# Kernel tuning notes

Measured on AMD Instinct MI355X. Metric: run time of the kernel, lower is better.

## Reference

```python
import jax, jax.numpy as jnp
import numpy as np

# DCNv2 config (matches init_kwargs)
STRIDE, PAD, DIL = 1, 1, 1
KH, KW = 3, 3
K = KH * KW


def setup_inputs() -> dict:
    key = jax.random.key(0)
    k1, k2, k3, k4 = jax.random.split(key, 4)
    B, C, H, W = 2, 256, 96, 96
    O = 256
    inp = jax.random.normal(k1, (B, C, H, W), jnp.float32)
    # offset channels interleaved (dy, dx) per kernel tap -> 2*K channels
    offset = jax.random.normal(k2, (B, 2 * K, H, W), jnp.float32)
    # modulation mask in [0,1) (sigmoid is applied outside this module in DCN heads)
    mask = jax.random.uniform(k3, (B, K, H, W), jnp.float32)
    n = C * KH * KW
    stdv = 1.0 / float(np.sqrt(n))
    weight = jax.random.uniform(k4, (O, C, KH, KW), jnp.float32, -stdv, stdv)
    bias = jnp.zeros((O,), jnp.float32)
    return {"input": inp, "offset": offset, "mask": mask, "weight": weight, "bias": bias}


def reference(input, offset, mask, weight, bias):
    B, C, H, W = input.shape
    O = weight.shape[0]
    Ho = (H + 2 * PAD - DIL * (KH - 1) - 1) // STRIDE + 1
    Wo = (W + 2 * PAD - DIL * (KW - 1) - 1) // STRIDE + 1

    # learned per-pixel offsets: channel layout [dy_k0, dx_k0, dy_k1, dx_k1, ...]
    dy = offset[:, 0::2]  # [B,K,Ho,Wo]
    dx = offset[:, 1::2]  # [B,K,Ho,Wo]

    ky = (jnp.arange(K) // KW * DIL).astype(jnp.float32)  # kernel tap row offsets
    kx = (jnp.arange(K) % KW * DIL).astype(jnp.float32)   # kernel tap col offsets
    base_y = (jnp.arange(Ho) * STRIDE - PAD).astype(jnp.float32)
    base_x = (jnp.arange(Wo) * STRIDE - PAD).astype(jnp.float32)

    # sampling positions, [B,K,Ho,Wo]
    y = base_y[None, None, :, None] + ky[None, :, None, None] + dy
    x = base_x[None, None, None, :] + kx[None, :, None, None] + dx

    y0 = jnp.floor(y)
    x0 = jnp.floor(x)
    wy = y - y0  # bilinear fractional weights
    wx = x - x0

    inp_flat = input.reshape(B, C, H * W)

    def gather(yi, xi):
        # zero-padded bilinear corner gather: out-of-bounds -> 0
        ii = yi.astype(jnp.int32)
        jj = xi.astype(jnp.int32)
        valid = ((ii >= 0) & (ii < H) & (jj >= 0) & (jj < W)).astype(input.dtype)
        idx = jnp.clip(ii, 0, H - 1) * W + jnp.clip(jj, 0, W - 1)  # [B,K,Ho,Wo]
        v = jnp.take_along_axis(inp_flat, idx.reshape(B, 1, -1), axis=2)  # [B,C,K*Ho*Wo]
        return v * valid.reshape(B, 1, -1)

    v00 = gather(y0, x0)
    v01 = gather(y0, x0 + 1)
    v10 = gather(y0 + 1, x0)
    v11 = gather(y0 + 1, x0 + 1)

    wyf = wy.reshape(B, 1, -1)
    wxf = wx.reshape(B, 1, -1)
    sampled = (v00 * (1 - wyf) * (1 - wxf) + v01 * (1 - wyf) * wxf
               + v10 * wyf * (1 - wxf) + v11 * wyf * wxf)  # [B,C,K*Ho*Wo]

    mod = sampled * mask.reshape(B, 1, -1)           # modulation per tap/pixel
    mod = mod.reshape(B, C, K, Ho * Wo)
    out = jnp.einsum('bcks,ock->bos', mod, weight.reshape(O, C, K)) + bias[None, :, None]
    return out.reshape(B, O, Ho, Wo)
```

## Files before the change

kernel.cpp:

```cpp
#include <hip/hip_runtime.h>
#include <hip/hip_bf16.h>


#define Hh 96
#define Ww 96
#define Cc 256
#define Oo 256
#define Bb 2
#define Kk 9
#define Ss (Hh * Ww)
#define CKTOT (Cc * Kk)

typedef __bf16 bf16x8 __attribute__((ext_vector_type(8)));
typedef __bf16 bf16x2v __attribute__((ext_vector_type(2)));
typedef float f32x16 __attribute__((ext_vector_type(16)));
typedef float f32x2 __attribute__((ext_vector_type(2)));

__device__ __forceinline__ f32x2 up2(unsigned u) {
  f32x2 r;
  r.x = __uint_as_float(u << 16);
  r.y = __uint_as_float(u & 0xffff0000u);
  return r;
}

__device__ __forceinline__ void barrier_lgkm() {
  asm volatile("" ::: "memory");
  __builtin_amdgcn_s_waitcnt(0xC07F);
  __builtin_amdgcn_s_barrier();
  asm volatile("" ::: "memory");
}

__global__ __launch_bounds__(256) void prep(const float* __restrict__ inp,
                                            const float* __restrict__ wsrc,
                                            __bf16* __restrict__ it,
                                            __bf16* __restrict__ wt) {
  __shared__ float tile[64][65];
  const int bx = blockIdx.x;
  const int tid = threadIdx.x;

  if (bx < 1152) {
    const int hw0 = (bx % 144) * 64;
    const int c0 = ((bx / 144) & 3) * 64;
    const int b = bx / 576;
    const int hw_l = tid & 63, cr = tid >> 6;
    const float* src = inp + ((size_t)(b * Cc + c0) * Ss) + hw0;
#pragma unroll
    for (int r = 0; r < 16; ++r) {
      int c_l = r * 4 + cr;
      tile[c_l][hw_l] = src[(size_t)c_l * Ss + hw_l];
    }
    __syncthreads();
    const int cp = (tid & 31) * 2, hr = tid >> 5;
    __bf16* dst = it + ((size_t)(b * Ss + hw0) * Cc) + c0;
#pragma unroll
    for (int r = 0; r < 8; ++r) {
      int hw_s = r * 8 + hr;
      bf16x2v p;
      p.x = (__bf16)tile[cp][hw_s];
      p.y = (__bf16)tile[cp + 1][hw_s];
      *(bf16x2v*)(dst + (size_t)hw_s * Cc + cp) = p;
    }
  } else {
    int i = (bx - 1152) * 256 + tid;
    int j = i & 7;
    int l = (i >> 3) & 63;
    int osub = (i >> 9) & 7;
    int cc = (i >> 12) & 15;
    int kk = i >> 16;
    int o = osub * 32 + (l & 31);
    int ch = cc * 16 + ((l >> 5) << 3) + j;
    wt[i] = (__bf16)wsrc[(o * Cc + ch) * Kk + kk];
  }
}

__global__ __launch_bounds__(256, 3) void dcn_main(
    const __bf16* __restrict__ it,
    const __bf16* __restrict__ wt,
    const float* __restrict__ offset,
    const float* __restrict__ mask,
    const float* __restrict__ bias,
    float* __restrict__ out)
{
  __shared__ __bf16 colT[2][32 * 256];
  __shared__ int4 pa9[9][32];
  __shared__ float4 pw9[9][32];

  const int tid = threadIdx.x;
  const int tile = (blockIdx.x & 7) * 36 + (blockIdx.x >> 3);
  const int s0 = tile * 32;
  const int b = blockIdx.y;
  const int lane = tid & 63;
  const int wv = tid >> 6;
  const int sB = lane & 31;
  const int hi = lane >> 5;
  const int fs = tid >> 3;
  const int fg = tid & 7;

  const __bf16* itb = it + (size_t)b * Ss * Cc;

  for (int idx = tid; idx < 9 * 32; idx += 256) {
    int kk = idx >> 5;
    int sl = idx & 31;
    int s = s0 + sl;
    int ho = s / Ww;
    int wo = s - ho * Ww;
    float dy = offset[((size_t)(b * 18 + 2 * kk)) * Ss + s];
    float dx = offset[((size_t)(b * 18 + 2 * kk + 1)) * Ss + s];
    float m = mask[((size_t)(b * 9 + kk)) * Ss + s];
    float y = (float)(ho - 1 + kk / 3) + dy;
    float x = (float)(wo - 1 + kk % 3) + dx;
    float fy = floorf(y), fx = floorf(x);
    int y0 = (int)fy, x0 = (int)fx;
    float wy = y - fy, wx = x - fx;
    int y1 = y0 + 1, x1 = x0 + 1;
    float vy0 = (y0 >= 0 && y0 < Hh) ? 1.f : 0.f;
    float vy1 = (y1 >= 0 && y1 < Hh) ? 1.f : 0.f;
    float vx0 = (x0 >= 0 && x0 < Ww) ? 1.f : 0.f;
    float vx1 = (x1 >= 0 && x1 < Ww) ? 1.f : 0.f;
    int y0c = min(max(y0, 0), Hh - 1), y1c = min(max(y1, 0), Hh - 1);
    int x0c = min(max(x0, 0), Ww - 1), x1c = min(max(x1, 0), Ww - 1);
    pa9[kk][sl] = make_int4((y0c * Ww + x0c) * Cc, (y0c * Ww + x1c) * Cc,
                            (y1c * Ww + x0c) * Cc, (y1c * Ww + x1c) * Cc);
    pw9[kk][sl] = make_float4(m * (1.f - wy) * (1.f - wx) * vy0 * vx0,
                              m * (1.f - wy) * wx * vy0 * vx1,
                              m * wy * (1.f - wx) * vy1 * vx0,
                              m * wy * wx * vy1 * vx1);
  }
  __syncthreads();

  f32x16 acc0, acc1;
#pragma unroll
  for (int j = 0; j < 16; ++j) { acc0[j] = 0.f; acc1[j] = 0.f; }

  auto ldW = [&](int kk, int cc, int which) {
    size_t idx = (size_t)((kk * 16 + cc) * 8 + wv * 2 + which);
    return *(const bf16x8*)(wt + (idx << 9) + (lane << 3));
  };
  auto ldB = [&](int buf, int cc) {
    int g = ((2 * cc + hi) ^ (sB & 7)) << 3;
    return *(const bf16x8*)(&colT[buf][sB * 256 + g]);
  };

  for (int kk = 0; kk < Kk; ++kk) {
    const int buf = kk & 1;
    {
      int4 a = pa9[kk][fs];
      float4 wq = pw9[kk][fs];
      __bf16* drow = &colT[buf][fs * 256];
#pragma unroll
      for (int it2 = 0; it2 < 4; ++it2) {
        int g = fg + it2 * 8;
        const __bf16* p = itb + g * 8;
        uint4 c00 = *(const uint4*)(p + a.x);
        uint4 c01 = *(const uint4*)(p + a.y);
        uint4 c10 = *(const uint4*)(p + a.z);
        uint4 c11 = *(const uint4*)(p + a.w);
        unsigned u0[4] = {c00.x, c00.y, c00.z, c00.w};
        unsigned u1[4] = {c01.x, c01.y, c01.z, c01.w};
        unsigned u2[4] = {c10.x, c10.y, c10.z, c10.w};
        unsigned u3[4] = {c11.x, c11.y, c11.z, c11.w};
        bf16x8 rv;
#pragma unroll
        for (int w = 0; w < 4; ++w) {
          f32x2 r = up2(u0[w]) * wq.x + up2(u1[w]) * wq.y +
                    up2(u2[w]) * wq.z + up2(u3[w]) * wq.w;
          rv[2 * w] = (__bf16)r.x;
          rv[2 * w + 1] = (__bf16)r.y;
        }
        *(bf16x8*)(drow + ((g ^ (fs & 7)) << 3)) = rv;
      }
    }
    bf16x8 Wacur = ldW(kk, 0, 0);
    bf16x8 Wbcur = ldW(kk, 0, 1);
    barrier_lgkm();

    bf16x8 Bcur = ldB(buf, 0);
#pragma unroll
    for (int cc = 0; cc < 16; ++cc) {
      bf16x8 Bn, Wan, Wbn;
      if (cc < 15) {
        Bn = ldB(buf, cc + 1);
        Wan = ldW(kk, cc + 1, 0);
        Wbn = ldW(kk, cc + 1, 1);
      }
      acc0 = __builtin_amdgcn_mfma_f32_32x32x16_bf16(Wacur, Bcur, acc0, 0, 0, 0);
      acc1 = __builtin_amdgcn_mfma_f32_32x32x16_bf16(Wbcur, Bcur, acc1, 0, 0, 0);
      if (cc < 15) {
        Bcur = Bn;
        Wacur = Wan;
        Wbcur = Wbn;
      }
    }
  }

  float* ob = out + (size_t)b * Oo * Ss + s0 + sB;
#pragma unroll
  for (int os = 0; os < 2; ++os) {
#pragma unroll
    for (int r = 0; r < 16; ++r) {
      int o = wv * 64 + os * 32 + (r & 3) + 8 * (r >> 2) + 4 * hi;
      float v = (os ? acc1[r] : acc0[r]) + bias[o];
      ob[(size_t)o * Ss] = v;
    }
  }
}

extern "C" void kernel_launch(void* const* d_in, const int* in_sizes, int n_in,
                              void* d_out, int out_size, void* d_ws, size_t ws_size,
                              hipStream_t stream) {
  (void)in_sizes; (void)n_in; (void)out_size; (void)ws_size;
  const float* inp = (const float*)d_in[0];
  const float* offset = (const float*)d_in[1];
  const float* mask = (const float*)d_in[2];
  const float* weight = (const float*)d_in[3];
  const float* bias = (const float*)d_in[4];
  float* out = (float*)d_out;

  __bf16* it = (__bf16*)d_ws;
  __bf16* wt = (__bf16*)((char*)d_ws + (size_t)Bb * Ss * Cc * 2);

  prep<<<3456, 256, 0, stream>>>(inp, weight, it, wt);
  dcn_main<<<dim3(288, Bb), 256, 0, stream>>>(it, wt, offset, mask, bias, out);
}
```

Measured before the change: 128.1 us.

## Software-pipeline bilinear gather of next tap with MFMA of current tap

Restructures the main loop so the bilinear gather and blend for tap kk+1 is issued in two halves, interleaved with the MFMA chain for tap kk, writing into the other LDS buffer. This hides global gather latency behind matrix math and removes the per-tap serialization of gather then compute. Operand prefetch depth for weights and B fragments is raised to three steps ahead. Occupancy is dropped from 3 to 2 waves per SIMD to make room for the extra live registers, which could reduce latency hiding elsewhere.

```diff
diff --git a/kernel.cpp b/kernel.cpp
--- a/kernel.cpp
+++ b/kernel.cpp
@@ -73,7 +73,42 @@
   }
 }
 
-__global__ __launch_bounds__(256, 3) void dcn_main(
+__device__ __forceinline__ void issue_half(const __bf16* __restrict__ itb,
+                                           const int4 a, int fg, int h,
+                                           uint4 (&c)[2][4]) {
+#pragma unroll
+  for (int t = 0; t < 2; ++t) {
+    const __bf16* p = itb + (fg + (h * 2 + t) * 8) * 8;
+    c[t][0] = *(const uint4*)(p + a.x);
+    c[t][1] = *(const uint4*)(p + a.y);
+    c[t][2] = *(const uint4*)(p + a.z);
+    c[t][3] = *(const uint4*)(p + a.w);
+  }
+}
+
+__device__ __forceinline__ void proc_half(const float4 wq, int fg, int fs, int h,
+                                          const uint4 (&c)[2][4],
+                                          __bf16* __restrict__ drow) {
+#pragma unroll
+  for (int t = 0; t < 2; ++t) {
+    int g = fg + (h * 2 + t) * 8;
+    unsigned u0[4] = {c[t][0].x, c[t][0].y, c[t][0].z, c[t][0].w};
+    unsigned u1[4] = {c[t][1].x, c[t][1].y, c[t][1].z, c[t][1].w};
+    unsigned u2[4] = {c[t][2].x, c[t][2].y, c[t][2].z, c[t][2].w};
+    unsigned u3[4] = {c[t][3].x, c[t][3].y, c[t][3].z, c[t][3].w};
+    bf16x8 rv;
+#pragma unroll
+    for (int w = 0; w < 4; ++w) {
+      f32x2 r = up2(u0[w]) * wq.x + up2(u1[w]) * wq.y +
+                up2(u2[w]) * wq.z + up2(u3[w]) * wq.w;
+      rv[2 * w] = (__bf16)r.x;
+      rv[2 * w + 1] = (__bf16)r.y;
+    }
+    *(bf16x8*)(drow + ((g ^ (fs & 7)) << 3)) = rv;
+  }
+}
+
+__global__ __launch_bounds__(256, 2) void dcn_main(
     const __bf16* __restrict__ it,
     const __bf16* __restrict__ wt,
     const float* __restrict__ offset,
@@ -141,57 +176,66 @@
     return *(const bf16x8*)(&colT[buf][sB * 256 + g]);
   };
 
+  bf16x8 Wa[4], Wb[4], Bv[4];
+  uint4 cA[2][4], cB[2][4];
+
+  {
+    int4 a0 = pa9[0][fs];
+    float4 w0 = pw9[0][fs];
+    issue_half(itb, a0, fg, 0, cA);
+    issue_half(itb, a0, fg, 1, cB);
+    proc_half(w0, fg, fs, 0, cA, &colT[0][fs * 256]);
+    proc_half(w0, fg, fs, 1, cB, &colT[0][fs * 256]);
+  }
+  Wa[0] = ldW(0, 0, 0); Wb[0] = ldW(0, 0, 1);
+  Wa[1] = ldW(0, 1, 0); Wb[1] = ldW(0, 1, 1);
+  barrier_lgkm();
+
+#define STEP(cc)                                                               \
+  {                                                                            \
+    if ((cc) < 13) {                                                           \
+      Wa[((cc) + 3) & 3] = ldW(kk, (cc) + 3, 0);                               \
+      Wb[((cc) + 3) & 3] = ldW(kk, (cc) + 3, 1);                               \
+      Bv[((cc) + 3) & 3] = ldB(buf, (cc) + 3);                                 \
+    }                                                                          \
+    acc0 = __builtin_amdgcn_mfma_f32_32x32x16_bf16(Wa[(cc) & 3], Bv[(cc) & 3], \
+                                                   acc0, 0, 0, 0);             \
+    acc1 = __builtin_amdgcn_mfma_f32_32x32x16_bf16(Wb[(cc) & 3], Bv[(cc) & 3], \
+                                                   acc1, 0, 0, 0);             \
+  }
+
   for (int kk = 0; kk < Kk; ++kk) {
     const int buf = kk & 1;
-    {
-      int4 a = pa9[kk][fs];
-      float4 wq = pw9[kk][fs];
-      __bf16* drow = &colT[buf][fs * 256];
-#pragma unroll
-      for (int it2 = 0; it2 < 4; ++it2) {
-        int g = fg + it2 * 8;
-        const __bf16* p = itb + g * 8;
-        uint4 c00 = *(const uint4*)(p + a.x);
-        uint4 c01 = *(const uint4*)(p + a.y);
-        uint4 c10 = *(const uint4*)(p + a.z);
-        uint4 c11 = *(const uint4*)(p + a.w);
-        unsigned u0[4] = {c00.x, c00.y, c00.z, c00.w};
-        unsigned u1[4] = {c01.x, c01.y, c01.z, c01.w};
-        unsigned u2[4] = {c10.x, c10.y, c10.z, c10.w};
-        unsigned u3[4] = {c11.x, c11.y, c11.z, c11.w};
-        bf16x8 rv;
-#pragma unroll
-        for (int w = 0; w < 4; ++w) {
-          f32x2 r = up2(u0[w]) * wq.x + up2(u1[w]) * wq.y +
-                    up2(u2[w]) * wq.z + up2(u3[w]) * wq.w;
-          rv[2 * w] = (__bf16)r.x;
-          rv[2 * w + 1] = (__bf16)r.y;
-        }
-        *(bf16x8*)(drow + ((g ^ (fs & 7)) << 3)) = rv;
-      }
-    }
-    bf16x8 Wacur = ldW(kk, 0, 0);
-    bf16x8 Wbcur = ldW(kk, 0, 1);
+    int4 na;
+    float4 nwq;
+    if (kk < 8) {
+      na = pa9[kk + 1][fs];
+      issue_half(itb, na, fg, 0, cA);
+    }
+    Bv[0] = ldB(buf, 0);
+    Bv[1] = ldB(buf, 1);
+    Bv[2] = ldB(buf, 2);
+    Wa[2] = ldW(kk, 2, 0);
+    Wb[2] = ldW(kk, 2, 1);
+
+    STEP(0) STEP(1) STEP(2) STEP(3) STEP(4) STEP(5) STEP(6) STEP(7)
+
+    if (kk < 8) {
+      nwq = pw9[kk + 1][fs];
+      proc_half(nwq, fg, fs, 0, cA, &colT[buf ^ 1][fs * 256]);
+      issue_half(itb, na, fg, 1, cB);
+    }
+
+    STEP(8) STEP(9) STEP(10) STEP(11) STEP(12) STEP(13) STEP(14) STEP(15)
+
+    if (kk < 8) {
+      proc_half(nwq, fg, fs, 1, cB, &colT[buf ^ 1][fs * 256]);
+      Wa[0] = ldW(kk + 1, 0, 0); Wb[0] = ldW(kk + 1, 0, 1);
+      Wa[1] = ldW(kk + 1, 1, 0); Wb[1] = ldW(kk + 1, 1, 1);
+    }
     barrier_lgkm();
-
-    bf16x8 Bcur = ldB(buf, 0);
-#pragma unroll
-    for (int cc = 0; cc < 16; ++cc) {
-      bf16x8 Bn, Wan, Wbn;
-      if (cc < 15) {
-        Bn = ldB(buf, cc + 1);
-        Wan = ldW(kk, cc + 1, 0);
-        Wbn = ldW(kk, cc + 1, 1);
-      }
-      acc0 = __builtin_amdgcn_mfma_f32_32x32x16_bf16(Wacur, Bcur, acc0, 0, 0, 0);
-      acc1 = __builtin_amdgcn_mfma_f32_32x32x16_bf16(Wbcur, Bcur, acc1, 0, 0, 0);
-      if (cc < 15) {
-        Bcur = Bn;
-        Wacur = Wan;
-        Wbcur = Wbn;
-      }
-    }
-  }
+  }
+#undef STEP
 
   float* ob = out + (size_t)b * Oo * Ss + s0 + sB;
 #pragma unroll
```

After: 131.6 us. 1.03x slower.

## Split channel reduction across two wave groups with 512-thread blocks

Applied to the files above, without the earlier changes.

The main kernel now launches 512 threads per block. Two groups of four waves each handle half of the channel chunks in the MFMA loop, and each thread gathers half as many channel groups. The second group's partial accumulators are reduced through shared memory (reusing colT) before the first group writes the output. This raises the number of waves available to hide gather and MFMA latency, at the cost of an extra LDS reduction, two added barriers and doubled per-block thread pressure.

```diff
diff --git a/kernel.cpp b/kernel.cpp
--- a/kernel.cpp
+++ b/kernel.cpp
@@ -73,7 +73,7 @@
   }
 }
 
-__global__ __launch_bounds__(256, 3) void dcn_main(
+__global__ __launch_bounds__(512, 6) void dcn_main(
     const __bf16* __restrict__ it,
     const __bf16* __restrict__ wt,
     const float* __restrict__ offset,
@@ -91,16 +91,19 @@
   const int b = blockIdx.y;
   const int lane = tid & 63;
   const int wv = tid >> 6;
+  const int wq = wv & 3;
+  const int chh = wv >> 2;
+  const int cbase = chh * 8;
   const int sB = lane & 31;
   const int hi = lane >> 5;
-  const int fs = tid >> 3;
-  const int fg = tid & 7;
+  const int fs = tid >> 4;
+  const int fg = tid & 15;
 
   const __bf16* itb = it + (size_t)b * Ss * Cc;
 
-  for (int idx = tid; idx < 9 * 32; idx += 256) {
-    int kk = idx >> 5;
-    int sl = idx & 31;
+  if (tid < 9 * 32) {
+    int kk = tid >> 5;
+    int sl = tid & 31;
     int s = s0 + sl;
     int ho = s / Ww;
     int wo = s - ho * Ww;
@@ -133,7 +136,7 @@
   for (int j = 0; j < 16; ++j) { acc0[j] = 0.f; acc1[j] = 0.f; }
 
   auto ldW = [&](int kk, int cc, int which) {
-    size_t idx = (size_t)((kk * 16 + cc) * 8 + wv * 2 + which);
+    size_t idx = (size_t)((kk * 16 + cc) * 8 + wq * 2 + which);
     return *(const bf16x8*)(wt + (idx << 9) + (lane << 3));
   };
   auto ldB = [&](int buf, int cc) {
@@ -145,11 +148,11 @@
     const int buf = kk & 1;
     {
       int4 a = pa9[kk][fs];
-      float4 wq = pw9[kk][fs];
+      float4 wqv = pw9[kk][fs];
       __bf16* drow = &colT[buf][fs * 256];
 #pragma unroll
-      for (int it2 = 0; it2 < 4; ++it2) {
-        int g = fg + it2 * 8;
+      for (int it2 = 0; it2 < 2; ++it2) {
+        int g = fg + it2 * 16;
         const __bf16* p = itb + g * 8;
         uint4 c00 = *(const uint4*)(p + a.x);
         uint4 c01 = *(const uint4*)(p + a.y);
@@ -162,30 +165,30 @@
         bf16x8 rv;
 #pragma unroll
         for (int w = 0; w < 4; ++w) {
-          f32x2 r = up2(u0[w]) * wq.x + up2(u1[w]) * wq.y +
-                    up2(u2[w]) * wq.z + up2(u3[w]) * wq.w;
+          f32x2 r = up2(u0[w]) * wqv.x + up2(u1[w]) * wqv.y +
+                    up2(u2[w]) * wqv.z + up2(u3[w]) * wqv.w;
           rv[2 * w] = (__bf16)r.x;
           rv[2 * w + 1] = (__bf16)r.y;
         }
         *(bf16x8*)(drow + ((g ^ (fs & 7)) << 3)) = rv;
       }
     }
-    bf16x8 Wacur = ldW(kk, 0, 0);
-    bf16x8 Wbcur = ldW(kk, 0, 1);
+    bf16x8 Wacur = ldW(kk, cbase, 0);
+    bf16x8 Wbcur = ldW(kk, cbase, 1);
     barrier_lgkm();
 
-    bf16x8 Bcur = ldB(buf, 0);
-#pragma unroll
-    for (int cc = 0; cc < 16; ++cc) {
+    bf16x8 Bcur = ldB(buf, cbase);
+#pragma unroll
+    for (int cc = 0; cc < 8; ++cc) {
       bf16x8 Bn, Wan, Wbn;
-      if (cc < 15) {
-        Bn = ldB(buf, cc + 1);
-        Wan = ldW(kk, cc + 1, 0);
-        Wbn = ldW(kk, cc + 1, 1);
+      if (cc < 7) {
+        Bn = ldB(buf, cbase + cc + 1);
+        Wan = ldW(kk, cbase + cc + 1, 0);
+        Wbn = ldW(kk, cbase + cc + 1, 1);
       }
       acc0 = __builtin_amdgcn_mfma_f32_32x32x16_bf16(Wacur, Bcur, acc0, 0, 0, 0);
       acc1 = __builtin_amdgcn_mfma_f32_32x32x16_bf16(Wbcur, Bcur, acc1, 0, 0, 0);
-      if (cc < 15) {
+      if (cc < 7) {
         Bcur = Bn;
         Wacur = Wan;
         Wbcur = Wbn;
@@ -193,14 +196,28 @@
     }
   }
 
-  float* ob = out + (size_t)b * Oo * Ss + s0 + sB;
-#pragma unroll
-  for (int os = 0; os < 2; ++os) {
-#pragma unroll
-    for (int r = 0; r < 16; ++r) {
-      int o = wv * 64 + os * 32 + (r & 3) + 8 * (r >> 2) + 4 * hi;
-      float v = (os ? acc1[r] : acc0[r]) + bias[o];
-      ob[(size_t)o * Ss] = v;
+  __syncthreads();
+  float* red = (float*)colT;
+  if (chh == 1) {
+#pragma unroll
+    for (int os = 0; os < 2; ++os)
+#pragma unroll
+      for (int r = 0; r < 16; ++r)
+        red[(os * 16 + r) * 256 + wq * 64 + lane] = (os ? acc1[r] : acc0[r]);
+  }
+  __syncthreads();
+
+  if (chh == 0) {
+    float* ob = out + (size_t)b * Oo * Ss + s0 + sB;
+#pragma unroll
+    for (int os = 0; os < 2; ++os) {
+#pragma unroll
+      for (int r = 0; r < 16; ++r) {
+        int o = wq * 64 + os * 32 + (r & 3) + 8 * (r >> 2) + 4 * hi;
+        float v = (os ? acc1[r] : acc0[r]) +
+                  red[(os * 16 + r) * 256 + wq * 64 + lane] + bias[o];
+        ob[(size_t)o * Ss] = v;
+      }
     }
   }
 }
@@ -220,5 +237,5 @@
   __bf16* wt = (__bf16*)((char*)d_ws + (size_t)Bb * Ss * Cc * 2);
 
   prep<<<3456, 256, 0, stream>>>(inp, weight, it, wt);
-  dcn_main<<<dim3(288, Bb), 256, 0, stream>>>(it, wt, offset, mask, bias, out);
-}
+  dcn_main<<<dim3(288, Bb), 512, 0, stream>>>(it, wt, offset, mask, bias, out);
+}
```

Result: slower. 163.9 us (+28.0%).
